# Kernel tuning notes

Hardware: AMD Instinct MI355X
Metric: run time of the kernel (lower is better)

## Reference

```python
import jax, jax.numpy as jnp
import numpy as np
import math

B, S, D, H, N = 4, 2048, 1024, 8, 128  # batch, seq_len, d_model, n_heads, num_osc
ITERS = 10
DT = 0.1
PI = math.pi


def setup_inputs() -> dict:
    key = jax.random.key(0)
    ks = jax.random.split(key, 5)
    return {
        "x": jax.random.normal(ks[0], (B, S, D), jnp.float32),
        "mask": jnp.ones((B, S), jnp.int32),
        "W_phase": jax.random.normal(ks[1], (D, H * N), jnp.float32) / math.sqrt(D),
        "b_phase": jnp.zeros((H * N,), jnp.float32),
        "natural_freq": jax.random.normal(ks[2], (H, N), jnp.float32) * 0.1,
        "coupling": jnp.ones((H, 1, 1), jnp.float32),  # coupling_strength = 1.0
        "W_out": jax.random.normal(ks[3], (H * N, D), jnp.float32) / math.sqrt(H * N),
        "b_out": jnp.zeros((D,), jnp.float32),
    }


def reference(x, mask, W_phase, b_phase, natural_freq, coupling, W_out, b_out):
    # phases: [B, H, S, N]
    ph = (x @ W_phase + b_phase).reshape(B, S, H, N).transpose(0, 2, 1, 3)
    ph = jnp.tanh(ph) * PI
    m = mask.astype(ph.dtype)[:, None, :, None]  # [B,1,S,1] mask over j
    K = coupling.reshape(1, H, 1, 1)
    w = natural_freq.reshape(1, H, 1, N)

    def step(ph, _):
        s = jnp.sin(ph)
        c = jnp.cos(ph)
        # mean_j m_j * sin(theta_i - theta_j) = sin(th_i)*mean(m*cos) - cos(th_i)*mean(m*sin)
        ms = (m * s).mean(axis=2, keepdims=True)  # [B,H,1,N]
        mc = (m * c).mean(axis=2, keepdims=True)
        dtheta = w + K * (s * mc - c * ms)
        ph2 = jnp.mod(ph + DT * dtheta + PI, 2 * PI) - PI
        return ph2, None

    ph, _ = jax.lax.scan(step, ph, None, length=ITERS)
    # from_phase; dropout is identity in eval mode
    y = ph.transpose(0, 2, 1, 3).reshape(B, S, H * N) @ W_out + b_out
    return y
```

## Files before the change

### kernel.cpp

```cpp
#include <hip/hip_runtime.h>
#include <math.h>

#define S_ 2048
#define D_ 1024
#define HN_ 1024
#define B_ 4
#define M_ 8192
#define ITERS_ 10
#define DT_ 0.1f
#define PI_ 3.14159265358979323846f
#define TWOPI_ 6.28318530717958647692f
#define INV2PI_ 0.15915494309189533577f
#define SCALE_ 4096.0f
#define INVSC2_ (1.0f / 16777216.0f)

typedef __attribute__((ext_vector_type(8))) _Float16 f16x8;
typedef __attribute__((ext_vector_type(4))) float f32x4;

__device__ __align__(16) ushort g_xs [(size_t)M_ * 2048];
__device__ __align__(16) ushort g_WpT[(size_t)HN_ * 2048];
__device__ __align__(16) ushort g_WoT[(size_t)D_ * 1024];
__device__ __align__(16) float  g_ph [(size_t)B_ * HN_ * S_];
__device__ __align__(16) ushort g_phh[(size_t)B_ * HN_ * S_];
__device__ __align__(16) ushort g_phT[(size_t)M_ * HN_];

__device__ __forceinline__ ushort f2h(float f) {
    union { _Float16 h; ushort u; } v; v.h = (_Float16)f; return v.u;
}
__device__ __forceinline__ void split2s(float x, ushort& A, ushort& Bc) {
    const float xs = x * SCALE_;
    union { _Float16 h; ushort u; } va, vb;
    va.h = (_Float16)xs;
    const float r = xs - (float)va.h;
    vb.h = (_Float16)r;
    A = va.u; Bc = vb.u;
}
__device__ __forceinline__ void gload16(const void* g, void* l) {
    __builtin_amdgcn_global_load_lds(
        (const __attribute__((address_space(1))) void*)g,
        (__attribute__((address_space(3))) void*)l, 16, 0, 0);
}
__device__ __forceinline__ int pack2(ushort a, ushort b) {
    return (int)(unsigned)a | ((int)(unsigned)b << 16);
}

__global__ __launch_bounds__(256) void split_x(const float* __restrict__ X) {
    const int idx = blockIdx.x * 256 + threadIdx.x;
    const float4 v = ((const float4*)X)[idx];
    const int m  = idx >> 8;
    const int k4 = (idx & 255) * 4;
    ushort a[4], b[4];
    split2s(v.x, a[0], b[0]);
    split2s(v.y, a[1], b[1]);
    split2s(v.z, a[2], b[2]);
    split2s(v.w, a[3], b[3]);
    ushort* row = g_xs + (size_t)m * 2048 + k4;
    int2 oa; oa.x = pack2(a[0], a[1]); oa.y = pack2(a[2], a[3]);
    int2 ob; ob.x = pack2(b[0], b[1]); ob.y = pack2(b[2], b[3]);
    *(int2*)(row)        = oa;
    *(int2*)(row + 1024) = ob;
}

__global__ __launch_bounds__(256) void splitT_Wp(const float* __restrict__ Wp) {
    __shared__ float t[64][68];
    const int k0 = blockIdx.x * 64;
    const int n0 = blockIdx.y * 64;
    const int r = threadIdx.x >> 2;
    const int c = (threadIdx.x & 3) * 16;
    const float* src = Wp + (size_t)(k0 + r) * HN_ + n0 + c;
    #pragma unroll
    for (int q = 0; q < 4; ++q)
        *(float4*)&t[r][c + 4 * q] = ((const float4*)src)[q];
    __syncthreads();
    ushort ha[16], hb[16];
    #pragma unroll
    for (int j = 0; j < 16; ++j)
        split2s(t[c + j][r], ha[j], hb[j]);
    int4 a0, a1, b0, b1;
    a0.x = pack2(ha[0], ha[1]);   a0.y = pack2(ha[2], ha[3]);
    a0.z = pack2(ha[4], ha[5]);   a0.w = pack2(ha[6], ha[7]);
    a1.x = pack2(ha[8], ha[9]);   a1.y = pack2(ha[10], ha[11]);
    a1.z = pack2(ha[12], ha[13]); a1.w = pack2(ha[14], ha[15]);
    b0.x = pack2(hb[0], hb[1]);   b0.y = pack2(hb[2], hb[3]);
    b0.z = pack2(hb[4], hb[5]);   b0.w = pack2(hb[6], hb[7]);
    b1.x = pack2(hb[8], hb[9]);   b1.y = pack2(hb[10], hb[11]);
    b1.z = pack2(hb[12], hb[13]); b1.w = pack2(hb[14], hb[15]);
    ushort* dst = g_WpT + (size_t)(n0 + r) * 2048 + k0 + c;
    *(int4*)(dst)        = a0; *(int4*)(dst + 8)    = a1;
    *(int4*)(dst + 1024) = b0; *(int4*)(dst + 1032) = b1;
}

__global__ __launch_bounds__(256) void castT_Wo(const float* __restrict__ Wo) {
    __shared__ float t[64][68];
    const int k0 = blockIdx.x * 64;
    const int n0 = blockIdx.y * 64;
    const int r = threadIdx.x >> 2;
    const int c = (threadIdx.x & 3) * 16;
    const float* src = Wo + (size_t)(k0 + r) * D_ + n0 + c;
    #pragma unroll
    for (int q = 0; q < 4; ++q)
        *(float4*)&t[r][c + 4 * q] = ((const float4*)src)[q];
    __syncthreads();
    ushort h[16];
    #pragma unroll
    for (int j = 0; j < 16; ++j) h[j] = f2h(t[c + j][r]);
    ushort* dst = g_WoT + (size_t)(n0 + r) * 1024 + k0 + c;
    int4 o0, o1;
    o0.x = pack2(h[0], h[1]);   o0.y = pack2(h[2], h[3]);
    o0.z = pack2(h[4], h[5]);   o0.w = pack2(h[6], h[7]);
    o1.x = pack2(h[8], h[9]);   o1.y = pack2(h[10], h[11]);
    o1.z = pack2(h[12], h[13]); o1.w = pack2(h[14], h[15]);
    *(int4*)dst = o0;
    *(int4*)(dst + 8) = o1;
}

template<int NT, int SPLIT>
__device__ __forceinline__ void gemm_mainloop(const ushort* __restrict__ A,
                                              const ushort* __restrict__ Bm,
                                              ushort* lds,
                                              int m0, int n0, int tid,
                                              f32x4 (&acc)[4][4]) {
    constexpr int KROW = SPLIT ? 2048 : 1024;
    const int l   = tid & 63, wid = tid >> 6;
    const int wm  = wid >> 1, wn = wid & 1;
    const int l15 = l & 15, h = l >> 4;
    const int row4 = tid >> 2;
    const int soff = ((tid & 3) ^ (row4 & 3)) << 4;
    const char* gA = (const char*)(A + (size_t)m0 * KROW);
    const char* gB = (const char*)(Bm + (size_t)n0 * KROW);
    const int rdA = (wm * 64 + l15) * 64 + ((h ^ (l15 & 3)) << 4);
    const int rdB = 8192 + (wn * 64 + l15) * 64 + ((h ^ (l15 & 3)) << 4);

    #define AOFF(T) ((SPLIT && (T) >= 64) ? 2048 + ((T) - 64) * 64 : ((T) & 31) * 64)
    #define BOFF(T) (SPLIT ? ((T) < 32 ? (T) * 64 : ((T) < 64 ? 2048 + ((T) - 32) * 64 \
                                                              : ((T) - 64) * 64)) : (T) * 64)

    #define STAGE(T, BUF) do {                                                    \
        const int ao_ = AOFF(T), bo_ = BOFF(T);                                   \
        char* lb_ = (char*)lds + (BUF) * 16384;                                   \
        gload16(gA + (size_t)(row4)      * (KROW * 2) + ao_ + soff, lb_ + tid * 16);          \
        gload16(gA + (size_t)(row4 + 64) * (KROW * 2) + ao_ + soff, lb_ + 4096 + tid * 16);   \
        gload16(gB + (size_t)(row4)      * (KROW * 2) + bo_ + soff, lb_ + 8192 + tid * 16);   \
        gload16(gB + (size_t)(row4 + 64) * (KROW * 2) + bo_ + soff, lb_ + 12288 + tid * 16);  \
    } while (0)

    #define SB __builtin_amdgcn_sched_barrier(0)

    STAGE(0, 0);

    #pragma unroll 2
    for (int t = 0; t < NT; ++t) {
        SB; __builtin_amdgcn_s_barrier(); SB;
        if (t + 1 < NT) {
            STAGE(t + 1, (t + 1) & 1);
            asm volatile("s_waitcnt vmcnt(4)" ::: "memory");
        } else {
            asm volatile("s_waitcnt vmcnt(0)" ::: "memory");
        }
        SB; __builtin_amdgcn_s_barrier(); SB;

        const char* bb = (const char*)lds + (t & 1) * 16384;
        f16x8 Aa[4], Bb[4];
        #pragma unroll
        for (int i = 0; i < 4; ++i) Aa[i] = *(const f16x8*)(bb + rdA + i * 1024);
        #pragma unroll
        for (int j = 0; j < 4; ++j) Bb[j] = *(const f16x8*)(bb + rdB + j * 1024);
        __builtin_amdgcn_s_setprio(1);
        #pragma unroll
        for (int i = 0; i < 4; ++i)
            #pragma unroll
            for (int j = 0; j < 4; ++j)
                acc[i][j] = __builtin_amdgcn_mfma_f32_16x16x32_f16(
                    Aa[i], Bb[j], acc[i][j], 0, 0, 0);
        __builtin_amdgcn_s_setprio(0);
    }
    #undef STAGE
    #undef SB
    #undef AOFF
    #undef BOFF
}

__device__ __forceinline__ void tile_map(int bid, int& m0, int& n0) {
    const int xcd = bid & 7;
    const int idx = bid >> 3;
    m0 = (xcd * 8 + (idx >> 3)) * 128;
    n0 = (idx & 7) * 128;
}

__global__ __launch_bounds__(256, 4) void gemm1(const float* __restrict__ bias) {
    __shared__ ushort lds[2 * 8192];
    const int tid = threadIdx.x;
    int m0, n0;
    tile_map(blockIdx.x, m0, n0);
    const int wid = tid >> 6, l = tid & 63;
    const int wm = wid >> 1, wn = wid & 1;

    f32x4 acc[4][4];
    #pragma unroll
    for (int i = 0; i < 4; ++i)
        #pragma unroll
        for (int j = 0; j < 4; ++j) acc[i][j] = (f32x4){0.f, 0.f, 0.f, 0.f};

    gemm_mainloop<96, 1>(g_xs, g_WpT, lds, m0, n0, tid, acc);

    const int r4 = (l >> 4) * 4;
    const int cn = l & 15;
    #pragma unroll
    for (int i = 0; i < 4; ++i) {
        const int mg = m0 + wm * 64 + i * 16 + r4;
        const int bidx = mg >> 11;
        const int sg = mg & 2047;
        #pragma unroll
        for (int jj = 0; jj < 4; ++jj) {
            const int ng = n0 + wn * 64 + jj * 16 + cn;
            const float bb = bias[ng];
            float4 o;
            o.x = PI_ * tanhf(fmaf(acc[i][jj][0], INVSC2_, bb));
            o.y = PI_ * tanhf(fmaf(acc[i][jj][1], INVSC2_, bb));
            o.z = PI_ * tanhf(fmaf(acc[i][jj][2], INVSC2_, bb));
            o.w = PI_ * tanhf(fmaf(acc[i][jj][3], INVSC2_, bb));
            *(float4*)(g_ph + ((size_t)bidx * HN_ + ng) * S_ + sg) = o;
        }
    }
}

__global__ __launch_bounds__(256, 4) void gemm3(const float* __restrict__ bias,
                                                float* __restrict__ Y) {
    __shared__ ushort lds[2 * 8192];
    const int tid = threadIdx.x;
    int m0, n0;
    tile_map(blockIdx.x, m0, n0);
    const int wid = tid >> 6, l = tid & 63;
    const int wm = wid >> 1, wn = wid & 1;

    f32x4 acc[4][4];
    #pragma unroll
    for (int i = 0; i < 4; ++i)
        #pragma unroll
        for (int j = 0; j < 4; ++j) acc[i][j] = (f32x4){0.f, 0.f, 0.f, 0.f};

    gemm_mainloop<32, 0>(g_phT, g_WoT, lds, m0, n0, tid, acc);

    const int r4 = (l >> 4) * 4;
    const int cn = l & 15;
    #pragma unroll
    for (int i = 0; i < 4; ++i) {
        const int mg = m0 + wm * 64 + i * 16 + r4;
        #pragma unroll
        for (int jj = 0; jj < 4; ++jj) {
            const int ng = n0 + wn * 64 + jj * 16 + cn;
            const float bb = bias[ng];
            #pragma unroll
            for (int r = 0; r < 4; ++r)
                Y[(size_t)(mg + r) * D_ + ng] = acc[i][jj][r] + bb;
        }
    }
}

__global__ __launch_bounds__(256) void kuramoto(const int* __restrict__ mask,
                                                const float* __restrict__ natf,
                                                const float* __restrict__ coup) {
    const int wave = blockIdx.x * 4 + (threadIdx.x >> 6);
    const int lane = threadIdx.x & 63;
    const int b = wave >> 10;
    const int hn = wave & 1023;
    const int h = hn >> 7;

    const float wf = natf[hn];
    const float K = coup[h];

    const float* base = g_ph + ((size_t)b * HN_ + hn) * S_;

    float ph[32];
    #pragma unroll
    for (int i = 0; i < 8; ++i) {
        float4 v = *(const float4*)(base + i * 256 + lane * 4);
        ph[4 * i + 0] = v.x; ph[4 * i + 1] = v.y;
        ph[4 * i + 2] = v.z; ph[4 * i + 3] = v.w;
    }

    const int* mb = mask + b * S_;
    unsigned mbits = 0;
    #pragma unroll
    for (int i = 0; i < 8; ++i) {
        int4 mv = *(const int4*)(mb + i * 256 + lane * 4);
        mbits |= (mv.x != 0 ? 1u : 0u) << (4 * i + 0);
        mbits |= (mv.y != 0 ? 1u : 0u) << (4 * i + 1);
        mbits |= (mv.z != 0 ? 1u : 0u) << (4 * i + 2);
        mbits |= (mv.w != 0 ? 1u : 0u) << (4 * i + 3);
    }

    for (int it = 0; it < ITERS_; ++it) {
        float s[32], c[32];
        float ls = 0.f, lc = 0.f;
        #pragma unroll
        for (int i = 0; i < 32; ++i) {
            s[i] = __sinf(ph[i]);
            c[i] = __cosf(ph[i]);
            const float mf = (float)((mbits >> i) & 1u);
            ls = fmaf(mf, s[i], ls);
            lc = fmaf(mf, c[i], lc);
        }
        #pragma unroll
        for (int off = 32; off; off >>= 1) {
            ls += __shfl_xor(ls, off);
            lc += __shfl_xor(lc, off);
        }
        const float ms = ls * (1.f / 2048.f);
        const float mc = lc * (1.f / 2048.f);
        #pragma unroll
        for (int i = 0; i < 32; ++i) {
            const float dth = fmaf(K, fmaf(s[i], mc, -c[i] * ms), wf);
            float t = fmaf(DT_, dth, ph[i]) + PI_;
            t -= TWOPI_ * floorf(t * INV2PI_);
            ph[i] = t - PI_;
        }
    }

    ushort* ob = g_phh + ((size_t)b * HN_ + hn) * S_;
    #pragma unroll
    for (int i = 0; i < 8; ++i) {
        ushort4 o;
        o.x = f2h(ph[4 * i + 0]); o.y = f2h(ph[4 * i + 1]);
        o.z = f2h(ph[4 * i + 2]); o.w = f2h(ph[4 * i + 3]);
        *(ushort4*)(ob + i * 256 + lane * 4) = o;
    }
}

__global__ __launch_bounds__(256) void transpose_ph() {
    __shared__ ushort t[64][72];
    const int b = blockIdx.z;
    const int h0 = blockIdx.y * 64;
    const int s0 = blockIdx.x * 64;
    const int r = threadIdx.x >> 2;
    const int c = (threadIdx.x & 3) * 16;
    const ushort* src = g_phh + ((size_t)b * HN_ + h0 + r) * S_ + s0 + c;
    *(int4*)&t[r][c] = *(const int4*)src;
    *(int4*)&t[r][c + 8] = *(const int4*)(src + 8);
    __syncthreads();
    ushort o[16];
    #pragma unroll
    for (int j = 0; j < 16; ++j) o[j] = t[c + j][r];
    ushort* dst = g_phT + ((size_t)(b * S_ + s0 + r)) * HN_ + h0 + c;
    int4 o0, o1;
    o0.x = pack2(o[0], o[1]);   o0.y = pack2(o[2], o[3]);
    o0.z = pack2(o[4], o[5]);   o0.w = pack2(o[6], o[7]);
    o1.x = pack2(o[8], o[9]);   o1.y = pack2(o[10], o[11]);
    o1.z = pack2(o[12], o[13]); o1.w = pack2(o[14], o[15]);
    *(int4*)dst = o0;
    *(int4*)(dst + 8) = o1;
}

extern "C" void kernel_launch(void* const* d_in, const int* in_sizes, int n_in,
                              void* d_out, int out_size, void* d_ws, size_t ws_size,
                              hipStream_t stream) {
    const float* x    = (const float*)d_in[0];
    const int*   mask = (const int*)d_in[1];
    const float* Wp   = (const float*)d_in[2];
    const float* bp   = (const float*)d_in[3];
    const float* natf = (const float*)d_in[4];
    const float* coup = (const float*)d_in[5];
    const float* Wo   = (const float*)d_in[6];
    const float* bo   = (const float*)d_in[7];
    float* y = (float*)d_out;

    split_x  <<<dim3(8192),         256, 0, stream>>>(x);
    splitT_Wp<<<dim3(16, 16),       256, 0, stream>>>(Wp);
    castT_Wo <<<dim3(16, 16),       256, 0, stream>>>(Wo);
    gemm1    <<<dim3(512),          256, 0, stream>>>(bp);
    kuramoto <<<dim3(1024),         256, 0, stream>>>(mask, natf, coup);
    transpose_ph<<<dim3(32, 16, 4), 256, 0, stream>>>();
    gemm3    <<<dim3(512),          256, 0, stream>>>(bo, y);
}
```

Baseline: 192.6 us.

## Split-K first GEMM, fuse prep kernels, retile second GEMM to 512 threads

The three preprocessing kernels are merged into one launch. The first GEMM is split along K into two halves, giving 1024 blocks instead of 512, and each half writes raw partial sums to its own fp32 buffer. The Kuramoto kernel now adds the two partials and applies bias, scale and tanh. The output GEMM uses 512-thread blocks with a 64-wide K tile, a different swizzle and 4x2 warp tiles. This trades an extra fp32 intermediate write and read for more parallelism and fewer launches.

```diff
diff --git a/kernel.cpp b/kernel.cpp
--- a/kernel.cpp
+++ b/kernel.cpp
@@ -20,7 +20,8 @@
 __device__ __align__(16) ushort g_xs [(size_t)M_ * 2048];
 __device__ __align__(16) ushort g_WpT[(size_t)HN_ * 2048];
 __device__ __align__(16) ushort g_WoT[(size_t)D_ * 1024];
-__device__ __align__(16) float  g_ph [(size_t)B_ * HN_ * S_];
+__device__ __align__(16) float  g_p0 [(size_t)B_ * HN_ * S_];
+__device__ __align__(16) float  g_p1 [(size_t)B_ * HN_ * S_];
 __device__ __align__(16) ushort g_phh[(size_t)B_ * HN_ * S_];
 __device__ __align__(16) ushort g_phT[(size_t)M_ * HN_];
 
@@ -44,127 +45,126 @@
     return (int)(unsigned)a | ((int)(unsigned)b << 16);
 }
 
-__global__ __launch_bounds__(256) void split_x(const float* __restrict__ X) {
-    const int idx = blockIdx.x * 256 + threadIdx.x;
-    const float4 v = ((const float4*)X)[idx];
-    const int m  = idx >> 8;
-    const int k4 = (idx & 255) * 4;
-    ushort a[4], b[4];
-    split2s(v.x, a[0], b[0]);
-    split2s(v.y, a[1], b[1]);
-    split2s(v.z, a[2], b[2]);
-    split2s(v.w, a[3], b[3]);
-    ushort* row = g_xs + (size_t)m * 2048 + k4;
-    int2 oa; oa.x = pack2(a[0], a[1]); oa.y = pack2(a[2], a[3]);
-    int2 ob; ob.x = pack2(b[0], b[1]); ob.y = pack2(b[2], b[3]);
-    *(int2*)(row)        = oa;
-    *(int2*)(row + 1024) = ob;
-}
-
-__global__ __launch_bounds__(256) void splitT_Wp(const float* __restrict__ Wp) {
+__global__ __launch_bounds__(256) void prep(const float* __restrict__ X,
+                                            const float* __restrict__ Wp,
+                                            const float* __restrict__ Wo) {
     __shared__ float t[64][68];
-    const int k0 = blockIdx.x * 64;
-    const int n0 = blockIdx.y * 64;
-    const int r = threadIdx.x >> 2;
-    const int c = (threadIdx.x & 3) * 16;
-    const float* src = Wp + (size_t)(k0 + r) * HN_ + n0 + c;
+    const int bid = blockIdx.x;
+    const int tid = threadIdx.x;
+    if (bid < 2048) {
+        #pragma unroll
+        for (int p = 0; p < 4; ++p) {
+            const int idx = bid * 1024 + p * 256 + tid;
+            const float4 v = ((const float4*)X)[idx];
+            const int m  = idx >> 8;
+            const int k4 = (idx & 255) * 4;
+            ushort a[4], b[4];
+            split2s(v.x, a[0], b[0]);
+            split2s(v.y, a[1], b[1]);
+            split2s(v.z, a[2], b[2]);
+            split2s(v.w, a[3], b[3]);
+            ushort* row = g_xs + (size_t)m * 2048 + k4;
+            int2 oa; oa.x = pack2(a[0], a[1]); oa.y = pack2(a[2], a[3]);
+            int2 ob; ob.x = pack2(b[0], b[1]); ob.y = pack2(b[2], b[3]);
+            *(int2*)(row)        = oa;
+            *(int2*)(row + 1024) = ob;
+        }
+        return;
+    }
+    const int wb   = bid - 2048;
+    const bool isWp = (wb < 256);
+    const int g  = isWp ? wb : wb - 256;
+    const int k0 = (g >> 4) * 64;
+    const int n0 = (g & 15) * 64;
+    const int r = tid >> 2;
+    const int c = (tid & 3) * 16;
+    const float* src = (isWp ? Wp : Wo) + (size_t)(k0 + r) * 1024 + n0 + c;
     #pragma unroll
     for (int q = 0; q < 4; ++q)
         *(float4*)&t[r][c + 4 * q] = ((const float4*)src)[q];
     __syncthreads();
-    ushort ha[16], hb[16];
-    #pragma unroll
-    for (int j = 0; j < 16; ++j)
-        split2s(t[c + j][r], ha[j], hb[j]);
-    int4 a0, a1, b0, b1;
-    a0.x = pack2(ha[0], ha[1]);   a0.y = pack2(ha[2], ha[3]);
-    a0.z = pack2(ha[4], ha[5]);   a0.w = pack2(ha[6], ha[7]);
-    a1.x = pack2(ha[8], ha[9]);   a1.y = pack2(ha[10], ha[11]);
-    a1.z = pack2(ha[12], ha[13]); a1.w = pack2(ha[14], ha[15]);
-    b0.x = pack2(hb[0], hb[1]);   b0.y = pack2(hb[2], hb[3]);
-    b0.z = pack2(hb[4], hb[5]);   b0.w = pack2(hb[6], hb[7]);
-    b1.x = pack2(hb[8], hb[9]);   b1.y = pack2(hb[10], hb[11]);
-    b1.z = pack2(hb[12], hb[13]); b1.w = pack2(hb[14], hb[15]);
-    ushort* dst = g_WpT + (size_t)(n0 + r) * 2048 + k0 + c;
-    *(int4*)(dst)        = a0; *(int4*)(dst + 8)    = a1;
-    *(int4*)(dst + 1024) = b0; *(int4*)(dst + 1032) = b1;
-}
-
-__global__ __launch_bounds__(256) void castT_Wo(const float* __restrict__ Wo) {
-    __shared__ float t[64][68];
-    const int k0 = blockIdx.x * 64;
-    const int n0 = blockIdx.y * 64;
-    const int r = threadIdx.x >> 2;
-    const int c = (threadIdx.x & 3) * 16;
-    const float* src = Wo + (size_t)(k0 + r) * D_ + n0 + c;
-    #pragma unroll
-    for (int q = 0; q < 4; ++q)
-        *(float4*)&t[r][c + 4 * q] = ((const float4*)src)[q];
-    __syncthreads();
-    ushort h[16];
-    #pragma unroll
-    for (int j = 0; j < 16; ++j) h[j] = f2h(t[c + j][r]);
-    ushort* dst = g_WoT + (size_t)(n0 + r) * 1024 + k0 + c;
-    int4 o0, o1;
-    o0.x = pack2(h[0], h[1]);   o0.y = pack2(h[2], h[3]);
-    o0.z = pack2(h[4], h[5]);   o0.w = pack2(h[6], h[7]);
-    o1.x = pack2(h[8], h[9]);   o1.y = pack2(h[10], h[11]);
-    o1.z = pack2(h[12], h[13]); o1.w = pack2(h[14], h[15]);
-    *(int4*)dst = o0;
-    *(int4*)(dst + 8) = o1;
-}
-
-template<int NT, int SPLIT>
-__device__ __forceinline__ void gemm_mainloop(const ushort* __restrict__ A,
-                                              const ushort* __restrict__ Bm,
-                                              ushort* lds,
-                                              int m0, int n0, int tid,
-                                              f32x4 (&acc)[4][4]) {
-    constexpr int KROW = SPLIT ? 2048 : 1024;
-    const int l   = tid & 63, wid = tid >> 6;
-    const int wm  = wid >> 1, wn = wid & 1;
-    const int l15 = l & 15, h = l >> 4;
-    const int row4 = tid >> 2;
-    const int soff = ((tid & 3) ^ (row4 & 3)) << 4;
-    const char* gA = (const char*)(A + (size_t)m0 * KROW);
-    const char* gB = (const char*)(Bm + (size_t)n0 * KROW);
-    const int rdA = (wm * 64 + l15) * 64 + ((h ^ (l15 & 3)) << 4);
-    const int rdB = 8192 + (wn * 64 + l15) * 64 + ((h ^ (l15 & 3)) << 4);
-
-    #define AOFF(T) ((SPLIT && (T) >= 64) ? 2048 + ((T) - 64) * 64 : ((T) & 31) * 64)
-    #define BOFF(T) (SPLIT ? ((T) < 32 ? (T) * 64 : ((T) < 64 ? 2048 + ((T) - 32) * 64 \
-                                                              : ((T) - 64) * 64)) : (T) * 64)
-
-    #define STAGE(T, BUF) do {                                                    \
-        const int ao_ = AOFF(T), bo_ = BOFF(T);                                   \
-        char* lb_ = (char*)lds + (BUF) * 16384;                                   \
-        gload16(gA + (size_t)(row4)      * (KROW * 2) + ao_ + soff, lb_ + tid * 16);          \
-        gload16(gA + (size_t)(row4 + 64) * (KROW * 2) + ao_ + soff, lb_ + 4096 + tid * 16);   \
-        gload16(gB + (size_t)(row4)      * (KROW * 2) + bo_ + soff, lb_ + 8192 + tid * 16);   \
-        gload16(gB + (size_t)(row4 + 64) * (KROW * 2) + bo_ + soff, lb_ + 12288 + tid * 16);  \
+    if (isWp) {
+        ushort ha[16], hb[16];
+        #pragma unroll
+        for (int j = 0; j < 16; ++j)
+            split2s(t[c + j][r], ha[j], hb[j]);
+        int4 a0, a1, b0, b1;
+        a0.x = pack2(ha[0], ha[1]);   a0.y = pack2(ha[2], ha[3]);
+        a0.z = pack2(ha[4], ha[5]);   a0.w = pack2(ha[6], ha[7]);
+        a1.x = pack2(ha[8], ha[9]);   a1.y = pack2(ha[10], ha[11]);
+        a1.z = pack2(ha[12], ha[13]); a1.w = pack2(ha[14], ha[15]);
+        b0.x = pack2(hb[0], hb[1]);   b0.y = pack2(hb[2], hb[3]);
+        b0.z = pack2(hb[4], hb[5]);   b0.w = pack2(hb[6], hb[7]);
+        b1.x = pack2(hb[8], hb[9]);   b1.y = pack2(hb[10], hb[11]);
+        b1.z = pack2(hb[12], hb[13]); b1.w = pack2(hb[14], hb[15]);
+        ushort* dst = g_WpT + (size_t)(n0 + r) * 2048 + k0 + c;
+        *(int4*)(dst)        = a0; *(int4*)(dst + 8)    = a1;
+        *(int4*)(dst + 1024) = b0; *(int4*)(dst + 1032) = b1;
+    } else {
+        ushort h[16];
+        #pragma unroll
+        for (int j = 0; j < 16; ++j) h[j] = f2h(t[c + j][r]);
+        ushort* dst = g_WoT + (size_t)(n0 + r) * 1024 + k0 + c;
+        int4 o0, o1;
+        o0.x = pack2(h[0], h[1]);   o0.y = pack2(h[2], h[3]);
+        o0.z = pack2(h[4], h[5]);   o0.w = pack2(h[6], h[7]);
+        o1.x = pack2(h[8], h[9]);   o1.y = pack2(h[10], h[11]);
+        o1.z = pack2(h[12], h[13]); o1.w = pack2(h[14], h[15]);
+        *(int4*)dst = o0;
+        *(int4*)(dst + 8) = o1;
+    }
+}
+
+template<int HALF>
+__device__ __forceinline__ void g1_loop(ushort* lds, int m0, int n0, int tid,
+                                        f32x4 (&acc)[4][4]) {
+    constexpr int NT = 48;
+    const int l = tid & 63, wid = tid >> 6;
+    const int wm = wid >> 1, wn = wid & 1;
+    const int srow  = tid >> 2;
+    const int sslot = ((tid & 3) ^ ((tid >> 3) & 3)) << 4;
+    const char* gA = (const char*)(g_xs + (size_t)m0 * 2048);
+    const char* gB = (const char*)(g_WpT + (size_t)n0 * 2048);
+    const int l15 = l & 15;
+    const int slotp = (((l >> 4) ^ ((l15 >> 1) & 3)) << 4);
+    const char* pA = (const char*)lds + (wm * 64 + l15) * 64 + slotp;
+    const char* pB = (const char*)lds + 8192 + (wn * 64 + l15) * 64 + slotp;
+
+    #define AOFFk(T) (HALF == 0 ? ((T) < 32 ? (T) * 64 : ((T) - 32) * 64)            \
+                                : ((T) < 16 ? 1024 + (T) * 64 : 2048 + ((T) - 16) * 64))
+    #define BOFFk(T) (HALF == 0 ? ((T) < 32 ? (T) * 64 : 2048 + ((T) - 32) * 64)     \
+                                : ((T) < 16 ? 3072 + (T) * 64 : ((T) - 16) * 64))
+
+    #define STAGE1(T, BUF) do {                                                      \
+        const int ao_ = AOFFk(T) + sslot, bo_ = BOFFk(T) + sslot;                    \
+        char* lb_ = (char*)lds + (BUF) * 16384 + wid * 1024;                         \
+        gload16(gA + (size_t)(srow)      * 4096 + ao_, lb_);                         \
+        gload16(gA + (size_t)(srow + 64) * 4096 + ao_, lb_ + 4096);                  \
+        gload16(gB + (size_t)(srow)      * 4096 + bo_, lb_ + 8192);                  \
+        gload16(gB + (size_t)(srow + 64) * 4096 + bo_, lb_ + 12288);                 \
     } while (0)
 
-    #define SB __builtin_amdgcn_sched_barrier(0)
-
-    STAGE(0, 0);
+    #define SB1 __builtin_amdgcn_sched_barrier(0)
+
+    STAGE1(0, 0);
 
     #pragma unroll 2
     for (int t = 0; t < NT; ++t) {
-        SB; __builtin_amdgcn_s_barrier(); SB;
+        SB1; __builtin_amdgcn_s_barrier(); SB1;
         if (t + 1 < NT) {
-            STAGE(t + 1, (t + 1) & 1);
+            STAGE1(t + 1, (t + 1) & 1);
             asm volatile("s_waitcnt vmcnt(4)" ::: "memory");
         } else {
             asm volatile("s_waitcnt vmcnt(0)" ::: "memory");
         }
-        SB; __builtin_amdgcn_s_barrier(); SB;
-
-        const char* bb = (const char*)lds + (t & 1) * 16384;
+        SB1; __builtin_amdgcn_s_barrier(); SB1;
+
+        const int bo = (t & 1) * 16384;
         f16x8 Aa[4], Bb[4];
         #pragma unroll
-        for (int i = 0; i < 4; ++i) Aa[i] = *(const f16x8*)(bb + rdA + i * 1024);
-        #pragma unroll
-        for (int j = 0; j < 4; ++j) Bb[j] = *(const f16x8*)(bb + rdB + j * 1024);
+        for (int i = 0; i < 4; ++i) Aa[i] = *(const f16x8*)(pA + bo + i * 1024);
+        #pragma unroll
+        for (int j = 0; j < 4; ++j) Bb[j] = *(const f16x8*)(pB + bo + j * 1024);
         __builtin_amdgcn_s_setprio(1);
         #pragma unroll
         for (int i = 0; i < 4; ++i)
@@ -174,35 +174,35 @@
                     Aa[i], Bb[j], acc[i][j], 0, 0, 0);
         __builtin_amdgcn_s_setprio(0);
     }
-    #undef STAGE
-    #undef SB
-    #undef AOFF
-    #undef BOFF
-}
-
-__device__ __forceinline__ void tile_map(int bid, int& m0, int& n0) {
+    #undef STAGE1
+    #undef SB1
+    #undef AOFFk
+    #undef BOFFk
+}
+
+__global__ __launch_bounds__(256, 4) void gemm1ks() {
+    __shared__ ushort lds[2 * 8192];
+    const int tid = threadIdx.x;
+    const int bid = blockIdx.x;
     const int xcd = bid & 7;
     const int idx = bid >> 3;
-    m0 = (xcd * 8 + (idx >> 3)) * 128;
-    n0 = (idx & 7) * 128;
-}
-
-__global__ __launch_bounds__(256, 4) void gemm1(const float* __restrict__ bias) {
-    __shared__ ushort lds[2 * 8192];
-    const int tid = threadIdx.x;
-    int m0, n0;
-    tile_map(blockIdx.x, m0, n0);
-    const int wid = tid >> 6, l = tid & 63;
+    const int m0 = (xcd * 8 + (idx >> 4)) * 128;
+    const int rest = idx & 15;
+    const int n0 = (rest >> 1) * 128;
+    const int half = rest & 1;
+
+    f32x4 acc[4][4];
+    #pragma unroll
+    for (int i = 0; i < 4; ++i)
+        #pragma unroll
+        for (int j = 0; j < 4; ++j) acc[i][j] = (f32x4){0.f, 0.f, 0.f, 0.f};
+
+    if (half == 0) g1_loop<0>(lds, m0, n0, tid, acc);
+    else           g1_loop<1>(lds, m0, n0, tid, acc);
+
+    float* pout = (half == 0) ? g_p0 : g_p1;
+    const int l = tid & 63, wid = tid >> 6;
     const int wm = wid >> 1, wn = wid & 1;
-
-    f32x4 acc[4][4];
-    #pragma unroll
-    for (int i = 0; i < 4; ++i)
-        #pragma unroll
-        for (int j = 0; j < 4; ++j) acc[i][j] = (f32x4){0.f, 0.f, 0.f, 0.f};
-
-    gemm_mainloop<96, 1>(g_xs, g_WpT, lds, m0, n0, tid, acc);
-
     const int r4 = (l >> 4) * 4;
     const int cn = l & 15;
     #pragma unroll
@@ -213,53 +213,15 @@
         #pragma unroll
         for (int jj = 0; jj < 4; ++jj) {
             const int ng = n0 + wn * 64 + jj * 16 + cn;
-            const float bb = bias[ng];
-            float4 o;
-            o.x = PI_ * tanhf(fmaf(acc[i][jj][0], INVSC2_, bb));
-            o.y = PI_ * tanhf(fmaf(acc[i][jj][1], INVSC2_, bb));
-            o.z = PI_ * tanhf(fmaf(acc[i][jj][2], INVSC2_, bb));
-            o.w = PI_ * tanhf(fmaf(acc[i][jj][3], INVSC2_, bb));
-            *(float4*)(g_ph + ((size_t)bidx * HN_ + ng) * S_ + sg) = o;
-        }
-    }
-}
-
-__global__ __launch_bounds__(256, 4) void gemm3(const float* __restrict__ bias,
-                                                float* __restrict__ Y) {
-    __shared__ ushort lds[2 * 8192];
-    const int tid = threadIdx.x;
-    int m0, n0;
-    tile_map(blockIdx.x, m0, n0);
-    const int wid = tid >> 6, l = tid & 63;
-    const int wm = wid >> 1, wn = wid & 1;
-
-    f32x4 acc[4][4];
-    #pragma unroll
-    for (int i = 0; i < 4; ++i)
-        #pragma unroll
-        for (int j = 0; j < 4; ++j) acc[i][j] = (f32x4){0.f, 0.f, 0.f, 0.f};
-
-    gemm_mainloop<32, 0>(g_phT, g_WoT, lds, m0, n0, tid, acc);
-
-    const int r4 = (l >> 4) * 4;
-    const int cn = l & 15;
-    #pragma unroll
-    for (int i = 0; i < 4; ++i) {
-        const int mg = m0 + wm * 64 + i * 16 + r4;
-        #pragma unroll
-        for (int jj = 0; jj < 4; ++jj) {
-            const int ng = n0 + wn * 64 + jj * 16 + cn;
-            const float bb = bias[ng];
-            #pragma unroll
-            for (int r = 0; r < 4; ++r)
-                Y[(size_t)(mg + r) * D_ + ng] = acc[i][jj][r] + bb;
-        }
-    }
-}
-
-__global__ __launch_bounds__(256) void kuramoto(const int* __restrict__ mask,
-                                                const float* __restrict__ natf,
-                                                const float* __restrict__ coup) {
+            *(f32x4*)(pout + ((size_t)bidx * HN_ + ng) * S_ + sg) = acc[i][jj];
+        }
+    }
+}
+
+__global__ __launch_bounds__(256) void kuramoto2(const int* __restrict__ mask,
+                                                 const float* __restrict__ natf,
+                                                 const float* __restrict__ coup,
+                                                 const float* __restrict__ bias) {
     const int wave = blockIdx.x * 4 + (threadIdx.x >> 6);
     const int lane = threadIdx.x & 63;
     const int b = wave >> 10;
@@ -268,15 +230,20 @@
 
     const float wf = natf[hn];
     const float K = coup[h];
-
-    const float* base = g_ph + ((size_t)b * HN_ + hn) * S_;
+    const float bb = bias[hn];
+
+    const float* p0 = g_p0 + ((size_t)b * HN_ + hn) * S_;
+    const float* p1 = g_p1 + ((size_t)b * HN_ + hn) * S_;
 
     float ph[32];
     #pragma unroll
     for (int i = 0; i < 8; ++i) {
-        float4 v = *(const float4*)(base + i * 256 + lane * 4);
-        ph[4 * i + 0] = v.x; ph[4 * i + 1] = v.y;
-        ph[4 * i + 2] = v.z; ph[4 * i + 3] = v.w;
+        float4 v0 = *(const float4*)(p0 + i * 256 + lane * 4);
+        float4 v1 = *(const float4*)(p1 + i * 256 + lane * 4);
+        ph[4 * i + 0] = PI_ * tanhf(fmaf(v0.x + v1.x, INVSC2_, bb));
+        ph[4 * i + 1] = PI_ * tanhf(fmaf(v0.y + v1.y, INVSC2_, bb));
+        ph[4 * i + 2] = PI_ * tanhf(fmaf(v0.z + v1.z, INVSC2_, bb));
+        ph[4 * i + 3] = PI_ * tanhf(fmaf(v0.w + v1.w, INVSC2_, bb));
     }
 
     const int* mb = mask + b * S_;
@@ -351,6 +318,109 @@
     *(int4*)(dst + 8) = o1;
 }
 
+__device__ __forceinline__ void g3_loop(ushort* lds, int m0, int n0, int tid,
+                                        f32x4 (&acc)[4][2]) {
+    constexpr int NT = 16;
+    const int l = tid & 63, wid = tid >> 6;
+    const int wm = wid >> 2, wn = wid & 3;
+    const int r8g  = l >> 3;
+    const int swzo = ((l & 7) * 16) ^ (r8g << 4);
+    const char* gA = (const char*)(g_phT + (size_t)m0 * 1024);
+    const char* gB = (const char*)(g_WoT + (size_t)n0 * 1024);
+    const int l15 = l & 15;
+    const int xk  = (l15 & 7) << 4;
+    const int sl0 = ((l >> 4) * 16) ^ xk;
+    const int sl1 = (64 + (l >> 4) * 16) ^ xk;
+    const char* pA = (const char*)lds + (wm * 64 + l15) * 128;
+    const char* pB = (const char*)lds + 16384 + (wn * 32 + l15) * 128;
+
+    #define STAGE3(T, BUF) do {                                                    \
+        const size_t gb_ = (size_t)(T) * 128 + swzo;                               \
+        char* lb_ = (char*)lds + (BUF) * 32768 + wid * 2048;                       \
+        gload16(gA + (size_t)(wid * 16 + r8g)     * 2048 + gb_, lb_);              \
+        gload16(gA + (size_t)(wid * 16 + 8 + r8g) * 2048 + gb_, lb_ + 1024);       \
+        gload16(gB + (size_t)(wid * 16 + r8g)     * 2048 + gb_, lb_ + 16384);      \
+        gload16(gB + (size_t)(wid * 16 + 8 + r8g) * 2048 + gb_, lb_ + 16384 + 1024); \
+    } while (0)
+
+    #define SB3 __builtin_amdgcn_sched_barrier(0)
+
+    STAGE3(0, 0);
+
+    #pragma unroll 2
+    for (int t = 0; t < NT; ++t) {
+        SB3; __builtin_amdgcn_s_barrier(); SB3;
+        if (t + 1 < NT) {
+            STAGE3(t + 1, (t + 1) & 1);
+            asm volatile("s_waitcnt vmcnt(4)" ::: "memory");
+        } else {
+            asm volatile("s_waitcnt vmcnt(0)" ::: "memory");
+        }
+        SB3; __builtin_amdgcn_s_barrier(); SB3;
+
+        const int bo = (t & 1) << 15;
+        f16x8 Aa[4][2], Bb[2][2];
+        #pragma unroll
+        for (int i = 0; i < 4; ++i) {
+            Aa[i][0] = *(const f16x8*)(pA + bo + i * 2048 + sl0);
+            Aa[i][1] = *(const f16x8*)(pA + bo + i * 2048 + sl1);
+        }
+        #pragma unroll
+        for (int j = 0; j < 2; ++j) {
+            Bb[j][0] = *(const f16x8*)(pB + bo + j * 2048 + sl0);
+            Bb[j][1] = *(const f16x8*)(pB + bo + j * 2048 + sl1);
+        }
+        __builtin_amdgcn_s_setprio(1);
+        #pragma unroll
+        for (int ks = 0; ks < 2; ++ks)
+            #pragma unroll
+            for (int i = 0; i < 4; ++i)
+                #pragma unroll
+                for (int j = 0; j < 2; ++j)
+                    acc[i][j] = __builtin_amdgcn_mfma_f32_16x16x32_f16(
+                        Aa[i][ks], Bb[j][ks], acc[i][j], 0, 0, 0);
+        __builtin_amdgcn_s_setprio(0);
+    }
+    #undef STAGE3
+    #undef SB3
+}
+
+__global__ __launch_bounds__(512, 4) void gemm3(const float* __restrict__ bias,
+                                                float* __restrict__ Y) {
+    __shared__ ushort lds[2 * 16384];
+    const int tid = threadIdx.x;
+    const int bid = blockIdx.x;
+    const int xcd = bid & 7;
+    const int idx = bid >> 3;
+    const int m0 = (xcd * 8 + (idx >> 3)) * 128;
+    const int n0 = (idx & 7) * 128;
+
+    f32x4 acc[4][2];
+    #pragma unroll
+    for (int i = 0; i < 4; ++i)
+        #pragma unroll
+        for (int j = 0; j < 2; ++j) acc[i][j] = (f32x4){0.f, 0.f, 0.f, 0.f};
+
+    g3_loop(lds, m0, n0, tid, acc);
+
+    const int l = tid & 63, wid = tid >> 6;
+    const int wm = wid >> 2, wn = wid & 3;
+    const int r4 = (l >> 4) * 4;
+    const int cn = l & 15;
+    #pragma unroll
+    for (int i = 0; i < 4; ++i) {
+        const int mg = m0 + wm * 64 + i * 16 + r4;
+        #pragma unroll
+        for (int jj = 0; jj < 2; ++jj) {
+            const int ng = n0 + wn * 32 + jj * 16 + cn;
+            const float bb = bias[ng];
+            #pragma unroll
+            for (int r = 0; r < 4; ++r)
+                Y[(size_t)(mg + r) * D_ + ng] = acc[i][jj][r] + bb;
+        }
+    }
+}
+
 extern "C" void kernel_launch(void* const* d_in, const int* in_sizes, int n_in,
                               void* d_out, int out_size, void* d_ws, size_t ws_size,
                               hipStream_t stream) {
@@ -364,11 +434,9 @@
     const float* bo   = (const float*)d_in[7];
     float* y = (float*)d_out;
 
-    split_x  <<<dim3(8192),         256, 0, stream>>>(x);
-    splitT_Wp<<<dim3(16, 16),       256, 0, stream>>>(Wp);
-    castT_Wo <<<dim3(16, 16),       256, 0, stream>>>(Wo);
-    gemm1    <<<dim3(512),          256, 0, stream>>>(bp);
-    kuramoto <<<dim3(1024),         256, 0, stream>>>(mask, natf, coup);
-    transpose_ph<<<dim3(32, 16, 4), 256, 0, stream>>>();
-    gemm3    <<<dim3(512),          256, 0, stream>>>(bo, y);
-}
+    prep        <<<dim3(2560),       256, 0, stream>>>(x, Wp, Wo);
+    gemm1ks     <<<dim3(1024),       256, 0, stream>>>();
+    kuramoto2   <<<dim3(1024),       256, 0, stream>>>(mask, natf, coup, bp);
+    transpose_ph<<<dim3(32, 16, 4),  256, 0, stream>>>();
+    gemm3       <<<dim3(512),        512, 0, stream>>>(bo, y);
+}
```

Result: faster. 188.2 us (-2.3%).
